# Kernel tuning notes

Measured on AMD Instinct MI355X. Metric: run time of the kernel, lower is better.

The kernel has to match this reference:

```python
import jax, jax.numpy as jnp
import numpy as np

B, SI, ST, D = 2, 1024, 512, 2048
H, KV, HD = 16, 4, 128
E, F, TOPK = 8, 1024, 2
EPS = 1e-6


def _rms(x, w):
    x32 = x.astype(jnp.float32)
    y = x32 * jax.lax.rsqrt(jnp.mean(x32 * x32, axis=-1, keepdims=True) + EPS)
    return y.astype(x.dtype) * w


def _rope(x, cos, sin):
    # x: [B,S,h,HD]; cos/sin: [S,HD//2]. Complex-pair rotation (use_real=False path):
    # pairs (x[2i], x[2i+1]) treated as complex, multiplied by e^{i theta}.
    xr, xi = x[..., 0::2], x[..., 1::2]
    c = cos[None, :, None, :]
    s = sin[None, :, None, :]
    out_r = xr * c - xi * s
    out_i = xr * s + xi * c
    return jnp.stack([out_r, out_i], axis=-1).reshape(x.shape)


def setup_inputs() -> dict:
    key = jax.random.key(0)
    ks = jax.random.split(key, 12)
    def w(k, shape, fan_in):
        return jax.random.normal(k, shape, jnp.float32) * (fan_in ** -0.5)
    pos_i = np.arange(SI)[:, None].astype(np.float32)
    pos_t = np.arange(ST)[:, None].astype(np.float32)
    inv = (1.0 / (10000.0 ** (np.arange(0, HD, 2).astype(np.float32) / HD)))[None, :]
    return {
        'hidden_states': jax.random.normal(ks[0], (B, SI, D), jnp.float32),
        'encoder_hidden_states': jax.random.normal(ks[1], (B, ST, D), jnp.float32),
        'img_cos': jnp.asarray(np.cos(pos_i * inv), jnp.float32),
        'img_sin': jnp.asarray(np.sin(pos_i * inv), jnp.float32),
        'txt_cos': jnp.asarray(np.cos(pos_t * inv), jnp.float32),
        'txt_sin': jnp.asarray(np.sin(pos_t * inv), jnp.float32),
        'norm1_w': jnp.ones((D,), jnp.float32),
        'norm2_w': jnp.ones((D,), jnp.float32),
        'wq': w(ks[2], (D, H * HD), D),
        'wk': w(ks[3], (D, KV * HD), D),
        'wv': w(ks[4], (D, KV * HD), D),
        'wk_txt': w(ks[5], (D, KV * HD), D),
        'wv_txt': w(ks[6], (D, KV * HD), D),
        'wo': w(ks[7], (H * HD, D), H * HD),
        'q_norm_w': jnp.ones((HD,), jnp.float32),
        'k_norm_w': jnp.ones((HD,), jnp.float32),
        'added_k_norm_w': jnp.ones((HD,), jnp.float32),
        'router_w': w(ks[8], (D, E), D),
        'gate_up_proj': w(ks[9], (E, D, 2 * F), D),
        'down_proj': w(ks[10], (E, F, D), F),
    }


def reference(hidden_states, encoder_hidden_states, img_cos, img_sin, txt_cos, txt_sin,
              norm1_w, norm2_w, wq, wk, wv, wk_txt, wv_txt, wo,
              q_norm_w, k_norm_w, added_k_norm_w, router_w, gate_up_proj, down_proj):
    h = hidden_states
    # ---- cross-attn: image queries over concat(image, text) K/V, GQA + RoPE ----
    x = _rms(h, norm1_w)
    q = _rms((x @ wq).reshape(B, SI, H, HD), q_norm_w)
    k_img = _rms((x @ wk).reshape(B, SI, KV, HD), k_norm_w)
    v_img = (x @ wv).reshape(B, SI, KV, HD)
    q = _rope(q, img_cos, img_sin)
    k_img = _rope(k_img, img_cos, img_sin)
    k_txt = _rms((encoder_hidden_states @ wk_txt).reshape(B, ST, KV, HD), added_k_norm_w)
    k_txt = _rope(k_txt, txt_cos, txt_sin)
    v_txt = (encoder_hidden_states @ wv_txt).reshape(B, ST, KV, HD)
    k = jnp.concatenate([k_img, k_txt], axis=1)  # [B, SI+ST, KV, HD]
    v = jnp.concatenate([v_img, v_txt], axis=1)
    k = jnp.repeat(k, H // KV, axis=2)  # GQA repeat_interleave over heads
    v = jnp.repeat(v, H // KV, axis=2)
    scores = jnp.einsum('bqhd,bkhd->bhqk', q, k) * (HD ** -0.5)
    attn = jax.nn.softmax(scores.astype(jnp.float32), axis=-1).astype(q.dtype)
    o = jnp.einsum('bhqk,bkhd->bqhd', attn, v).reshape(B, SI, H * HD)
    h = h + o @ wo
    # ---- MoE: top-k router + packed SwiGLU experts ----
    xt = _rms(h, norm2_w).reshape(B * SI, D)
    probs = jax.nn.softmax((xt @ router_w).astype(jnp.float32), axis=-1)
    topv, topi = jax.lax.top_k(probs, TOPK)
    topv = topv / jnp.sum(topv, axis=-1, keepdims=True)
    wgt = jnp.sum(jax.nn.one_hot(topi, E, dtype=xt.dtype) * topv.astype(xt.dtype)[..., None], axis=1)  # [T,E]
    gate_up = jnp.einsum('td,edg->teg', xt, gate_up_proj)  # [T,E,2F]
    gate, up = gate_up[..., :F], gate_up[..., F:]
    act = jax.nn.silu(gate) * up
    eo = jnp.einsum('tef,efd->ted', act, down_proj)  # [T,E,D]
    moe_out = jnp.einsum('te,ted->td', wgt, eo).reshape(B, SI, D)
    return h + moe_out
```

## Files before the change

kernel.cpp:

```cpp
#include <hip/hip_runtime.h>


typedef __attribute__((ext_vector_type(8))) __bf16 bf16x8;
typedef __attribute__((ext_vector_type(8))) unsigned short u16x8;
typedef __attribute__((ext_vector_type(4))) float f32x4;

__device__ __forceinline__ unsigned short f2bf(float x) {
  unsigned u = __builtin_bit_cast(unsigned, x);
  u += 0x7fffu + ((u >> 16) & 1u);
  return (unsigned short)(u >> 16);
}
__device__ __forceinline__ float bf2f(unsigned short b) {
  return __builtin_bit_cast(float, ((unsigned)b) << 16);
}

__device__ __forceinline__ void glds16(const unsigned short* g, unsigned short* l) {
  __builtin_amdgcn_global_load_lds(
      (const __attribute__((address_space(1))) void*)g,
      (__attribute__((address_space(3))) void*)l, 16, 0, 0);
}

__device__ __forceinline__ int xcd_swz(int orig, int nwg) {
  int q = nwg >> 3, r = nwg & 7;
  int xcd = orig & 7, idx = orig >> 3;
  int base = (xcd < r) ? xcd * (q + 1) : r * (q + 1) + (xcd - r) * q;
  return base + idx;
}

struct CvtJobs {
  const float* src[8];
  unsigned short* dst[8];
  int K[8];
  int N[8];
  int off[9];
};

__global__ __launch_bounds__(256) void convert_all(CvtJobs jb)
{
  __shared__ unsigned short T[64][66];
  const int bid = blockIdx.x;
  int j = 0;
  #pragma unroll
  for (int i = 0; i < 8; ++i) if (bid >= jb.off[i + 1]) j = i + 1;
  const int local = bid - jb.off[j];
  const int K = jb.K[j], N = jb.N[j];
  const int kb = K >> 6, nb = N >> 6;
  const int kt = local % kb;
  const int rest = local / kb;
  const int nt = rest % nb, zi = rest / nb;
  const float* Wz = jb.src[j] + (size_t)zi * K * N;
  unsigned short* WTz = jb.dst[j] + (size_t)zi * K * N;
  const int k0 = kt * 64, n0 = nt * 64;
  const int tid = threadIdx.x;
  #pragma unroll
  for (int i = tid; i < 64 * 16; i += 256) {
    int k = i >> 4, n4 = (i & 15) * 4;
    float4 v = *(const float4*)&Wz[(size_t)(k0 + k) * N + n0 + n4];
    T[n4 + 0][k] = f2bf(v.x);
    T[n4 + 1][k] = f2bf(v.y);
    T[n4 + 2][k] = f2bf(v.z);
    T[n4 + 3][k] = f2bf(v.w);
  }
  __syncthreads();
  #pragma unroll
  for (int i = tid; i < 64 * 8; i += 256) {
    int n = i >> 3, k8 = (i & 7) * 8;
    *(u16x8*)&WTz[(size_t)(n0 + n) * K + k0 + k8] = *(const u16x8*)&T[n][k8];
  }
}

struct Epi {
  unsigned short* qb;
  unsigned short* kbuf;
  unsigned short* vbuf;
  const float* q_nw;
  const float* k_nw;
  const float* kt_nw;
  const float* icos;
  const float* isin;
  const float* tcos;
  const float* tsin;
  float scale;
};

__global__ __launch_bounds__(256) void gemm_bb(
    const unsigned short* __restrict__ A, const unsigned short* __restrict__ BT,
    float* __restrict__ C, const float* __restrict__ resid,
    int M, int N, int K, int mode, Epi ep)
{
  __shared__ unsigned short As[2][128 * 64];
  __shared__ unsigned short Bs[2][128 * 64];
  const int mb = M >> 7;
  const int w = xcd_swz(blockIdx.x, gridDim.x);
  const int bm = (w % mb) * 128, bn = (w / mb) * 128;
  const int tid = threadIdx.x, lane = tid & 63, wid = tid >> 6;
  const int wm = (wid >> 1) * 64, wn = (wid & 1) * 64;
  const int l16 = lane & 15, g4 = lane >> 4;
  const int rseg = lane >> 3;
  const int csw  = ((lane & 7) ^ rseg) * 8;
  const unsigned short* aSrc[4];
  const unsigned short* bSrc[4];
  #pragma unroll
  for (int p = 0; p < 4; ++p) {
    int row = (p * 4 + wid) * 8 + rseg;
    aSrc[p] = A  + (size_t)(bm + row) * K + csw;
    bSrc[p] = BT + (size_t)(bn + row) * K + csw;
  }
  f32x4 acc[4][4] = {};
  const int NT = K >> 6;
  #pragma unroll
  for (int p = 0; p < 4; ++p) glds16(aSrc[p], &As[0][(p * 4 + wid) * 512]);
  #pragma unroll
  for (int p = 0; p < 4; ++p) glds16(bSrc[p], &Bs[0][(p * 4 + wid) * 512]);
  for (int t = 0; t < NT; ++t) {
    const int cur = t & 1;
    if (t + 1 < NT) {
      const int k0 = (t + 1) << 6;
      #pragma unroll
      for (int p = 0; p < 4; ++p) glds16(aSrc[p] + k0, &As[cur ^ 1][(p * 4 + wid) * 512]);
      #pragma unroll
      for (int p = 0; p < 4; ++p) glds16(bSrc[p] + k0, &Bs[cur ^ 1][(p * 4 + wid) * 512]);
      asm volatile("s_waitcnt vmcnt(8)" ::: "memory");
    } else {
      asm volatile("s_waitcnt vmcnt(0)" ::: "memory");
    }
    __builtin_amdgcn_s_barrier();
    __builtin_amdgcn_sched_barrier(0);
    const unsigned short* ab = &As[cur][0];
    const unsigned short* bb = &Bs[cur][0];
    #pragma unroll
    for (int ks = 0; ks < 2; ++ks) {
      bf16x8 af[4], bf[4];
      #pragma unroll
      for (int i = 0; i < 4; ++i) {
        int ra = wm + i * 16 + l16;
        int rb = wn + i * 16 + l16;
        int ch = ((ks * 4 + g4) ^ (l16 & 7)) * 8;
        af[i] = *(const bf16x8*)&ab[ra * 64 + ch];
        bf[i] = *(const bf16x8*)&bb[rb * 64 + ch];
      }
      #pragma unroll
      for (int mi = 0; mi < 4; ++mi)
        #pragma unroll
        for (int ni = 0; ni < 4; ++ni)
          acc[mi][ni] = __builtin_amdgcn_mfma_f32_16x16x32_bf16(af[mi], bf[ni], acc[mi][ni], 0, 0, 0);
    }
    __builtin_amdgcn_sched_barrier(0);
    __builtin_amdgcn_s_barrier();
  }
  const int r4 = g4 * 4;

  if (mode == 0) {
    #pragma unroll
    for (int mi = 0; mi < 4; ++mi)
      #pragma unroll
      for (int ni = 0; ni < 4; ++ni)
        #pragma unroll
        for (int r = 0; r < 4; ++r) {
          int row = bm + wm + mi * 16 + r4 + r;
          int col = bn + wn + ni * 16 + l16;
          float v = acc[mi][ni][r];
          if (resid) v += resid[(size_t)row * N + col];
          C[(size_t)row * N + col] = v;
        }
    return;
  }

  const int bt = bn >> 7;
  unsigned short* dst;
  const float* nw = nullptr;
  const float* cosT = nullptr;
  const float* sinT = nullptr;
  int h, NH, st, soff, vkind = 0, shift;
  float premul = 1.f;
  int S;
  if (mode == 1) {
    S = 1024; shift = 10;
    if (bt < 16)      { h = bt;      dst = ep.qb;   nw = ep.q_nw; cosT = ep.icos; sinT = ep.isin;
                        NH = 16; st = 1024; soff = 0; premul = ep.scale; }
    else if (bt < 20) { h = bt - 16; dst = ep.kbuf; nw = ep.k_nw; cosT = ep.icos; sinT = ep.isin;
                        NH = 4;  st = 1536; soff = 0; }
    else              { h = bt - 20; dst = ep.vbuf; vkind = 1; NH = 4; st = 1536; soff = 0; }
  } else {
    S = 512; shift = 9;
    if (bt < 4) { h = bt;     dst = ep.kbuf; nw = ep.kt_nw; cosT = ep.tcos; sinT = ep.tsin;
                  NH = 4; st = 1536; soff = 1024; }
    else        { h = bt - 4; dst = ep.vbuf; vkind = 1; NH = 4; st = 1536; soff = 1024; }
  }

  if (vkind) {
    #pragma unroll
    for (int mi = 0; mi < 4; ++mi)
      #pragma unroll
      for (int ni = 0; ni < 4; ++ni)
        #pragma unroll
        for (int r = 0; r < 4; ++r) {
          int row = wm + mi * 16 + r4 + r;
          int d   = wn + ni * 16 + l16;
          int token = bm + row;
          int srow = token & (S - 1), bidx = token >> shift;
          dst[((size_t)(bidx * NH + h) * st + srow + soff) * 128 + d] = f2bf(acc[mi][ni][r]);
        }
    return;
  }

  float* ssb = (float*)&As[0][0];
  float ssp[4][4];
  #pragma unroll
  for (int mi = 0; mi < 4; ++mi)
    #pragma unroll
    for (int r = 0; r < 4; ++r) {
      float v = 0.f;
      #pragma unroll
      for (int ni = 0; ni < 4; ++ni) v += acc[mi][ni][r] * acc[mi][ni][r];
      #pragma unroll
      for (int off = 1; off < 16; off <<= 1) v += __shfl_xor(v, off);
      ssp[mi][r] = v;
    }
  __syncthreads();
  if (l16 == 0) {
    #pragma unroll
    for (int mi = 0; mi < 4; ++mi)
      #pragma unroll
      for (int r = 0; r < 4; ++r)
        ssb[(wid & 1) * 128 + wm + mi * 16 + r4 + r] = ssp[mi][r];
  }
  __syncthreads();
  #pragma unroll
  for (int mi = 0; mi < 4; ++mi)
    #pragma unroll
    for (int r = 0; r < 4; ++r) {
      int row = wm + mi * 16 + r4 + r;
      float tot = ssb[row] + ssb[128 + row];
      float inv = rsqrtf(tot * (1.f / 128.f) + 1e-6f);
      int token = bm + row;
      int srow = token & (S - 1), bidx = token >> shift;
      #pragma unroll
      for (int ni = 0; ni < 4; ++ni) {
        int d = wn + ni * 16 + l16;
        float y = acc[mi][ni][r] * inv * nw[d];
        float part = __shfl_xor(y, 1);
        float c  = cosT[srow * 64 + (d >> 1)];
        float sn = sinT[srow * 64 + (d >> 1)];
        float outv = (d & 1) ? (part * sn + y * c) : (y * c - part * sn);
        dst[((size_t)(bidx * NH + h) * st + srow + soff) * 128 + d] = f2bf(outv * premul);
      }
    }
}

__global__ __launch_bounds__(512, 1) void gemm_moe_256sk(
    const unsigned short* __restrict__ A, const unsigned short* __restrict__ BTall,
    float* __restrict__ C0, float* __restrict__ C1,
    const int* __restrict__ counts, const int* __restrict__ offsets,
    const int* __restrict__ pair_token, const unsigned short* __restrict__ zbuf,
    int gather, int K, int N)
{
  const int w = xcd_swz(blockIdx.x, gridDim.x);
  const int e = w >> 7;
  const int local = w & 127;
  const int bm = ((local >> 4) & 7) * 256;
  const int kh = (local >> 3) & 1;
  const int bn = (local & 7) * 256;
  const int cnt = counts[e];
  if (bm >= cnt) return;
  const int base = offsets[e];
  const int Kh = K >> 1;
  float* __restrict__ C = kh ? C1 : C0;
  __shared__ unsigned short As[256 * 64];
  __shared__ unsigned short Bs[256 * 64];
  __shared__ int rowmap[256];
  const int tid = threadIdx.x, lane = tid & 63, wid = tid >> 6;
  const int wr = wid >> 2, wc = wid & 3;
  const int l16 = lane & 15, g4 = lane >> 4;
  const int rseg = lane >> 3;
  const int csw  = ((lane & 7) ^ rseg) * 8;
  if (tid < 256) {
    int lr = bm + tid;
    rowmap[tid] = (lr < cnt) ? (gather ? pair_token[base + lr] : base + lr) : -1;
  }
  __syncthreads();
  const unsigned short* BT = BTall + (size_t)e * N * K;
  const unsigned short* aSrc[4];
  const unsigned short* bSrc[4];
  int aOk[4];
  #pragma unroll
  for (int p = 0; p < 4; ++p) {
    int row = (p * 8 + wid) * 8 + rseg;
    int tok = rowmap[row];
    aOk[p] = (tok >= 0);
    aSrc[p] = aOk[p] ? (A + (size_t)tok * K + kh * Kh + csw) : (zbuf + csw);
    bSrc[p] = BT + (size_t)(bn + row) * K + kh * Kh + csw;
  }
  f32x4 acc[8][4] = {};
  const int NT = Kh >> 6;
  for (int t = 0; t < NT; ++t) {
    const int k0 = t << 6;
    #pragma unroll
    for (int p = 0; p < 4; ++p)
      glds16(aSrc[p] + (aOk[p] ? k0 : 0), &As[(p * 8 + wid) * 512]);
    #pragma unroll
    for (int p = 0; p < 4; ++p)
      glds16(bSrc[p] + k0, &Bs[(p * 8 + wid) * 512]);
    __syncthreads();
    #pragma unroll
    for (int ks = 0; ks < 2; ++ks) {
      const int ch = ((ks * 4 + g4) ^ (l16 & 7)) * 8;
      bf16x8 bf[4];
      #pragma unroll
      for (int j = 0; j < 4; ++j)
        bf[j] = *(const bf16x8*)&Bs[(wc * 64 + j * 16 + l16) * 64 + ch];
      #pragma unroll
      for (int mi = 0; mi < 8; ++mi) {
        bf16x8 af = *(const bf16x8*)&As[(wr * 128 + mi * 16 + l16) * 64 + ch];
        #pragma unroll
        for (int ni = 0; ni < 4; ++ni)
          acc[mi][ni] = __builtin_amdgcn_mfma_f32_16x16x32_bf16(af, bf[ni], acc[mi][ni], 0, 0, 0);
      }
    }
    __syncthreads();
  }
  const int r4 = g4 * 4;
  #pragma unroll
  for (int mi = 0; mi < 8; ++mi)
    #pragma unroll
    for (int ni = 0; ni < 4; ++ni)
      #pragma unroll
      for (int r = 0; r < 4; ++r) {
        int lrow = bm + wr * 128 + mi * 16 + r4 + r;
        int col  = bn + wc * 64 + ni * 16 + l16;
        if (lrow < cnt)
          C[(size_t)(base + lrow) * N + col] = acc[mi][ni][r];
      }
}

__global__ __launch_bounds__(256) void rmsnorm_rows(
    const float* __restrict__ in, const float* __restrict__ w,
    unsigned short* __restrict__ out)
{
  const int row = blockIdx.x;
  const int tid = threadIdx.x;
  const float* x = in + (size_t)row * 2048;
  float4 a = *(const float4*)&x[tid * 8];
  float4 b = *(const float4*)&x[tid * 8 + 4];
  float s = a.x*a.x + a.y*a.y + a.z*a.z + a.w*a.w
          + b.x*b.x + b.y*b.y + b.z*b.z + b.w*b.w;
  #pragma unroll
  for (int off = 1; off < 64; off <<= 1) s += __shfl_xor(s, off);
  __shared__ float red[4];
  if ((tid & 63) == 0) red[tid >> 6] = s;
  __syncthreads();
  float inv = rsqrtf((red[0] + red[1] + red[2] + red[3]) * (1.f / 2048.f) + 1e-6f);
  float4 wa = *(const float4*)&w[tid * 8];
  float4 wb = *(const float4*)&w[tid * 8 + 4];
  unsigned short* o = out + (size_t)row * 2048 + tid * 8;
  o[0] = f2bf(a.x * inv * wa.x); o[1] = f2bf(a.y * inv * wa.y);
  o[2] = f2bf(a.z * inv * wa.z); o[3] = f2bf(a.w * inv * wa.w);
  o[4] = f2bf(b.x * inv * wb.x); o[5] = f2bf(b.y * inv * wb.y);
  o[6] = f2bf(b.z * inv * wb.z); o[7] = f2bf(b.w * inv * wb.w);
}

__global__ __launch_bounds__(256) void rmsnorm_router(
    const float* __restrict__ in, const float* __restrict__ w,
    unsigned short* __restrict__ xt, const float* __restrict__ rw,
    int* __restrict__ topi, float* __restrict__ topw, int* __restrict__ counts)
{
  const int row = blockIdx.x;
  const int tid = threadIdx.x, lane = tid & 63, wid = tid >> 6;
  const float* x = in + (size_t)row * 2048;
  float4 a = *(const float4*)&x[tid * 8];
  float4 b = *(const float4*)&x[tid * 8 + 4];
  float s = a.x*a.x + a.y*a.y + a.z*a.z + a.w*a.w
          + b.x*b.x + b.y*b.y + b.z*b.z + b.w*b.w;
  #pragma unroll
  for (int off = 1; off < 64; off <<= 1) s += __shfl_xor(s, off);
  __shared__ float red[4];
  __shared__ float rl[4][8];
  if (lane == 0) red[wid] = s;
  __syncthreads();
  float inv = rsqrtf((red[0] + red[1] + red[2] + red[3]) * (1.f / 2048.f) + 1e-6f);
  float4 wa = *(const float4*)&w[tid * 8];
  float4 wb = *(const float4*)&w[tid * 8 + 4];
  float y[8] = {a.x * inv * wa.x, a.y * inv * wa.y, a.z * inv * wa.z, a.w * inv * wa.w,
                b.x * inv * wb.x, b.y * inv * wb.y, b.z * inv * wb.z, b.w * inv * wb.w};
  unsigned short* o = xt + (size_t)row * 2048 + tid * 8;
  #pragma unroll
  for (int j = 0; j < 8; ++j) o[j] = f2bf(y[j]);
  float lg[8] = {};
  #pragma unroll
  for (int j = 0; j < 8; ++j) {
    int d = tid * 8 + j;
    const float4 r0 = *(const float4*)&rw[d * 8];
    const float4 r1 = *(const float4*)&rw[d * 8 + 4];
    lg[0] += y[j] * r0.x; lg[1] += y[j] * r0.y; lg[2] += y[j] * r0.z; lg[3] += y[j] * r0.w;
    lg[4] += y[j] * r1.x; lg[5] += y[j] * r1.y; lg[6] += y[j] * r1.z; lg[7] += y[j] * r1.w;
  }
  #pragma unroll
  for (int e = 0; e < 8; ++e)
    #pragma unroll
    for (int off = 1; off < 64; off <<= 1) lg[e] += __shfl_xor(lg[e], off);
  if (lane == 0) {
    #pragma unroll
    for (int e = 0; e < 8; ++e) rl[wid][e] = lg[e];
  }
  __syncthreads();
  if (tid == 0) {
    float l[8];
    #pragma unroll
    for (int e = 0; e < 8; ++e) l[e] = rl[0][e] + rl[1][e] + rl[2][e] + rl[3][e];
    float v0 = l[0]; int e0 = 0;
    #pragma unroll
    for (int e = 1; e < 8; ++e) if (l[e] > v0) { v0 = l[e]; e0 = e; }
    float v1 = -1e30f; int e1 = 0;
    #pragma unroll
    for (int e = 0; e < 8; ++e) if (e != e0 && l[e] > v1) { v1 = l[e]; e1 = e; }
    float x1 = expf(v1 - v0);
    float w0 = 1.f / (1.f + x1);
    float w1 = x1 / (1.f + x1);
    topi[2 * row] = e0; topi[2 * row + 1] = e1;
    topw[2 * row] = w0; topw[2 * row + 1] = w1;
    atomicAdd(&counts[e0], 1);
    atomicAdd(&counts[e1], 1);
  }
}

__global__ __launch_bounds__(256) void f32_to_bf16_k(
    const float* __restrict__ in, unsigned short* __restrict__ out, int n)
{
  int i = (blockIdx.x * 256 + threadIdx.x) * 4;
  if (i + 3 < n) {
    float4 v = *(const float4*)&in[i];
    out[i + 0] = f2bf(v.x); out[i + 1] = f2bf(v.y);
    out[i + 2] = f2bf(v.z); out[i + 3] = f2bf(v.w);
  }
}

__global__ __launch_bounds__(512) void attn_kernel(
    const unsigned short* __restrict__ q,
    const unsigned short* __restrict__ kbuf,
    const unsigned short* __restrict__ vbuf,
    unsigned short* __restrict__ o)
{
  const int SK = 1536;
  const int w = xcd_swz(blockIdx.x, gridDim.x);
  const int bh = w >> 3;
  const int b = bh >> 4, h = bh & 15, kvh = h >> 2;
  const int q0 = (w & 7) * 128;
  const int tid = threadIdx.x, lane = tid & 63, wid = tid >> 6;
  const int l16 = lane & 15, kb = (lane >> 4) * 8, r4 = (lane >> 4) * 4;
  __shared__ unsigned short KsL[64 * 128];
  __shared__ unsigned short VTL[128 * 64];
  __shared__ unsigned short PsL[8 * 16 * 64];
  const int sr0 = tid >> 4;
  const int scc = (tid & 15) * 8;

  const unsigned short* qrow =
      q + ((size_t)(b * 16 + h) * 1024 + q0 + wid * 16 + l16) * 128;
  bf16x8 qf[4];
  #pragma unroll
  for (int ks = 0; ks < 4; ++ks) qf[ks] = *(const bf16x8*)&qrow[ks * 32 + kb];
  float mrow[4] = {-1e30f, -1e30f, -1e30f, -1e30f};
  float lrow[4] = {0.f, 0.f, 0.f, 0.f};
  f32x4 oacc[8] = {};
  const unsigned short* kb_base = kbuf + (size_t)(b * 4 + kvh) * SK * 128;
  const unsigned short* vb_base = vbuf + (size_t)(b * 4 + kvh) * SK * 128;

  u16x8 k0[2], v0[2], k1[2], v1[2];

#define ATT_LOAD(kr, vr, kt1)                                                 \
  {                                                                           \
    _Pragma("unroll")                                                         \
    for (int i = 0; i < 2; ++i) {                                             \
      kr[i] = *(const u16x8*)&kb_base[(size_t)((kt1) + sr0 + 32 * i) * 128 + scc]; \
      vr[i] = *(const u16x8*)&vb_base[(size_t)((kt1) + sr0 + 32 * i) * 128 + scc]; \
    }                                                                         \
  }

#define ATT_STAGE(kr, vr)                                                     \
  {                                                                           \
    _Pragma("unroll")                                                         \
    for (int i = 0; i < 2; ++i) {                                             \
      int rr = sr0 + 32 * i;                                                  \
      *(u16x8*)&KsL[rr * 128 + (((scc >> 3) ^ (rr & 7)) << 3)] = kr[i];       \
      _Pragma("unroll")                                                       \
      for (int j = 0; j < 8; ++j)                                             \
        VTL[(scc + j) * 64 + ((((rr >> 3) ^ ((scc + j) >> 3)) & 7) << 3) + (rr & 7)] = vr[i][j]; \
    }                                                                         \
  }

  auto compute = [&]() {
    f32x4 sacc[4] = {};
    __builtin_amdgcn_s_setprio(1);
    #pragma unroll
    for (int ks = 0; ks < 4; ++ks) {
      #pragma unroll
      for (int ni = 0; ni < 4; ++ni) {
        int rr = ni * 16 + l16;
        bf16x8 kf = *(const bf16x8*)
            &KsL[rr * 128 + ((((ks * 32 + kb) >> 3) ^ (rr & 7)) << 3)];
        sacc[ni] = __builtin_amdgcn_mfma_f32_16x16x32_bf16(qf[ks], kf, sacc[ni], 0, 0, 0);
      }
    }
    __builtin_amdgcn_s_setprio(0);
    float pv[4][4], alpha[4];
    #pragma unroll
    for (int r = 0; r < 4; ++r) {
      float tm = fmaxf(fmaxf(sacc[0][r], sacc[1][r]), fmaxf(sacc[2][r], sacc[3][r]));
      #pragma unroll
      for (int off = 1; off < 16; off <<= 1) tm = fmaxf(tm, __shfl_xor(tm, off));
      float mn = fmaxf(mrow[r], tm);
      alpha[r] = __expf(mrow[r] - mn);
      float s = 0.f;
      #pragma unroll
      for (int ni = 0; ni < 4; ++ni) {
        float p = __expf(sacc[ni][r] - mn);
        pv[ni][r] = p; s += p;
      }
      #pragma unroll
      for (int off = 1; off < 16; off <<= 1) s += __shfl_xor(s, off);
      lrow[r] = lrow[r] * alpha[r] + s;
      mrow[r] = mn;
    }
    #pragma unroll
    for (int ni = 0; ni < 8; ++ni)
      #pragma unroll
      for (int r = 0; r < 4; ++r) oacc[ni][r] *= alpha[r];
    #pragma unroll
    for (int ni = 0; ni < 4; ++ni)
      #pragma unroll
      for (int r = 0; r < 4; ++r) {
        int row = r4 + r, col = ni * 16 + l16;
        PsL[wid * 1024 + row * 64 + ((((col >> 3) ^ (row & 7)) & 7) << 3) + (col & 7)]
            = f2bf(pv[ni][r]);
      }
    asm volatile("s_waitcnt lgkmcnt(0)" ::: "memory");
    __builtin_amdgcn_sched_barrier(0);
    __builtin_amdgcn_s_setprio(1);
    #pragma unroll
    for (int ks = 0; ks < 2; ++ks) {
      bf16x8 pf = *(const bf16x8*)
          &PsL[wid * 1024 + l16 * 64 + ((((ks * 32 + kb) >> 3) ^ (l16 & 7)) << 3)];
      #pragma unroll
      for (int ni = 0; ni < 8; ++ni) {
        int d = ni * 16 + l16;
        bf16x8 vf = *(const bf16x8*)
            &VTL[d * 64 + ((((ks * 32 + kb) >> 3) ^ ((d >> 3) & 7)) << 3)];
        oacc[ni] = __builtin_amdgcn_mfma_f32_16x16x32_bf16(pf, vf, oacc[ni], 0, 0, 0);
      }
    }
    __builtin_amdgcn_s_setprio(0);
  };

  ATT_LOAD(k0, v0, 0);
  for (int t = 0; t < 24; t += 2) {
    ATT_STAGE(k0, v0);
    ATT_LOAD(k1, v1, (t + 1) * 64);
    asm volatile("s_waitcnt lgkmcnt(0)" ::: "memory");
    __builtin_amdgcn_s_barrier();
    __builtin_amdgcn_sched_barrier(0);
    compute();
    __builtin_amdgcn_sched_barrier(0);
    __builtin_amdgcn_s_barrier();
    ATT_STAGE(k1, v1);
    if (t + 2 < 24) ATT_LOAD(k0, v0, (t + 2) * 64);
    asm volatile("s_waitcnt lgkmcnt(0)" ::: "memory");
    __builtin_amdgcn_s_barrier();
    __builtin_amdgcn_sched_barrier(0);
    compute();
    __builtin_amdgcn_sched_barrier(0);
    __builtin_amdgcn_s_barrier();
  }
#undef ATT_LOAD
#undef ATT_STAGE

  #pragma unroll
  for (int ni = 0; ni < 8; ++ni)
    #pragma unroll
    for (int r = 0; r < 4; ++r) {
      float val = oacc[ni][r] / lrow[r];
      size_t row = (size_t)b * 1024 + q0 + wid * 16 + r4 + r;
      o[row * 2048 + h * 128 + ni * 16 + l16] = f2bf(val);
    }
}

__global__ void scan_offsets(const int* __restrict__ counts, int* __restrict__ offsets)
{
  if (threadIdx.x == 0 && blockIdx.x == 0) {
    int a = 0;
    for (int e = 0; e < 8; ++e) { offsets[e] = a; a += counts[e]; }
    offsets[8] = a;
  }
}

__global__ __launch_bounds__(256) void scatter_pairs(
    const int* __restrict__ topi, const int* __restrict__ offsets,
    int* __restrict__ fill, int* __restrict__ pair_token, int* __restrict__ token_slot)
{
  int t = blockIdx.x * 256 + threadIdx.x;
  if (t >= 2048) return;
  #pragma unroll
  for (int k = 0; k < 2; ++k) {
    int e = topi[2 * t + k];
    int slot = offsets[e] + atomicAdd(&fill[e], 1);
    pair_token[slot] = t;
    token_slot[2 * t + k] = slot;
  }
}

__global__ __launch_bounds__(256) void act_silu2(
    const float* __restrict__ gu0, const float* __restrict__ gu1,
    unsigned short* __restrict__ act)
{
  int p = blockIdx.x;
  int c = threadIdx.x * 4;
  float4 g0 = *(const float4*)&gu0[(size_t)p * 2048 + c];
  float4 g1 = *(const float4*)&gu1[(size_t)p * 2048 + c];
  float4 u0 = *(const float4*)&gu0[(size_t)p * 2048 + 1024 + c];
  float4 u1 = *(const float4*)&gu1[(size_t)p * 2048 + 1024 + c];
  float gg[4] = {g0.x + g1.x, g0.y + g1.y, g0.z + g1.z, g0.w + g1.w};
  float uu[4] = {u0.x + u1.x, u0.y + u1.y, u0.z + u1.z, u0.w + u1.w};
  #pragma unroll
  for (int j = 0; j < 4; ++j) {
    float a = gg[j] / (1.f + __expf(-gg[j])) * uu[j];
    act[(size_t)p * 1024 + c + j] = f2bf(a);
  }
}

__global__ __launch_bounds__(256) void moe_combine2(
    float* __restrict__ out, const float* __restrict__ eo0,
    const float* __restrict__ eo1,
    const int* __restrict__ token_slot, const float* __restrict__ topw)
{
  int t = blockIdx.x;
  int c = threadIdx.x * 8;
  int s0 = token_slot[2 * t], s1 = token_slot[2 * t + 1];
  float w0 = topw[2 * t], w1 = topw[2 * t + 1];
  #pragma unroll
  for (int j0 = 0; j0 < 8; j0 += 4) {
    float4 a0 = *(const float4*)&eo0[(size_t)s0 * 2048 + c + j0];
    float4 a1 = *(const float4*)&eo1[(size_t)s0 * 2048 + c + j0];
    float4 b0 = *(const float4*)&eo0[(size_t)s1 * 2048 + c + j0];
    float4 b1 = *(const float4*)&eo1[(size_t)s1 * 2048 + c + j0];
    float4 v = *(const float4*)&out[(size_t)t * 2048 + c + j0];
    v.x += w0 * (a0.x + a1.x) + w1 * (b0.x + b1.x);
    v.y += w0 * (a0.y + a1.y) + w1 * (b0.y + b1.y);
    v.z += w0 * (a0.z + a1.z) + w1 * (b0.z + b1.z);
    v.w += w0 * (a0.w + a1.w) + w1 * (b0.w + b1.w);
    *(float4*)&out[(size_t)t * 2048 + c + j0] = v;
  }
}

extern "C" void kernel_launch(void* const* d_in, const int* in_sizes, int n_in,
                              void* d_out, int out_size, void* d_ws, size_t ws_size,
                              hipStream_t stream)
{
  const float* hidden  = (const float*)d_in[0];
  const float* enc     = (const float*)d_in[1];
  const float* img_cos = (const float*)d_in[2];
  const float* img_sin = (const float*)d_in[3];
  const float* txt_cos = (const float*)d_in[4];
  const float* txt_sin = (const float*)d_in[5];
  const float* norm1_w = (const float*)d_in[6];
  const float* norm2_w = (const float*)d_in[7];
  const float* wq      = (const float*)d_in[8];
  const float* wk      = (const float*)d_in[9];
  const float* wv      = (const float*)d_in[10];
  const float* wk_txt  = (const float*)d_in[11];
  const float* wv_txt  = (const float*)d_in[12];
  const float* wo      = (const float*)d_in[13];
  const float* q_norm_w       = (const float*)d_in[14];
  const float* k_norm_w       = (const float*)d_in[15];
  const float* added_k_norm_w = (const float*)d_in[16];
  const float* router_w       = (const float*)d_in[17];
  const float* gate_up_proj   = (const float*)d_in[18];
  const float* down_proj      = (const float*)d_in[19];
  float* out = (float*)d_out;

  char* ws = (char*)d_ws;
  size_t off = 0;
  auto alloc = [&](size_t bytes) {
    void* p = ws + off;
    off += (bytes + 255) & ~(size_t)255;
    return p;
  };
  unsigned short* wqkvT  = (unsigned short*)alloc(3072ULL * 2048 * 2);
  unsigned short* wkvtT  = (unsigned short*)alloc(1024ULL * 2048 * 2);
  unsigned short* woT    = (unsigned short*)alloc(2048ULL * 2048 * 2);
  unsigned short* gupT   = (unsigned short*)alloc(8ULL * 2048 * 2048 * 2);
  unsigned short* dnT    = (unsigned short*)alloc(8ULL * 2048 * 1024 * 2);
  unsigned short* x_bf   = (unsigned short*)alloc(2048ULL * 2048 * 2);
  unsigned short* enc_bf = (unsigned short*)alloc(1024ULL * 2048 * 2);
  float* gu0  = (float*)alloc(4096ULL * 2048 * 4);
  float* gu1  = (float*)alloc(4096ULL * 2048 * 4);
  unsigned short* qb   = (unsigned short*)alloc(2048ULL * 2048 * 2);
  unsigned short* kbuf = (unsigned short*)alloc(2ULL * 4 * 1536 * 128 * 2);
  unsigned short* vbuf = (unsigned short*)alloc(2ULL * 4 * 1536 * 128 * 2);
  unsigned short* obuf = (unsigned short*)alloc(2048ULL * 2048 * 2);
  unsigned short* act  = obuf;
  unsigned short* xt   = (unsigned short*)alloc(2048ULL * 2048 * 2);
  int*   ctrl  = (int*)alloc(64 * sizeof(int));
  int*   topi  = (int*)alloc(4096 * 4);
  float* topw  = (float*)alloc(4096 * 4);
  int*   tslot = (int*)alloc(4096 * 4);
  int*   ptok  = (int*)alloc(4096 * 4);
  unsigned short* zbuf = (unsigned short*)alloc(256);
  int* counts = ctrl, * fill = ctrl + 8, * offsets = ctrl + 16;

  hipMemsetAsync(ctrl, 0, 64, stream);
  hipMemsetAsync(zbuf, 0, 256, stream);

  const float scale = 0.08838834764831845f;

  CvtJobs jb;
  jb.src[0] = wq;     jb.dst[0] = wqkvT;                  jb.K[0] = 2048; jb.N[0] = 2048;
  jb.src[1] = wk;     jb.dst[1] = wqkvT + 2048ULL * 2048; jb.K[1] = 2048; jb.N[1] = 512;
  jb.src[2] = wv;     jb.dst[2] = wqkvT + 2560ULL * 2048; jb.K[2] = 2048; jb.N[2] = 512;
  jb.src[3] = wk_txt; jb.dst[3] = wkvtT;                  jb.K[3] = 2048; jb.N[3] = 512;
  jb.src[4] = wv_txt; jb.dst[4] = wkvtT + 512ULL * 2048;  jb.K[4] = 2048; jb.N[4] = 512;
  jb.src[5] = wo;     jb.dst[5] = woT;                    jb.K[5] = 2048; jb.N[5] = 2048;
  jb.src[6] = gate_up_proj; jb.dst[6] = gupT;             jb.K[6] = 2048; jb.N[6] = 2048;
  jb.src[7] = down_proj;    jb.dst[7] = dnT;              jb.K[7] = 1024; jb.N[7] = 2048;
  jb.off[0] = 0;     jb.off[1] = 1024;  jb.off[2] = 1280; jb.off[3] = 1536;
  jb.off[4] = 1792;  jb.off[5] = 2048;  jb.off[6] = 3072; jb.off[7] = 11264;
  jb.off[8] = 15360;
  convert_all<<<15360, 256, 0, stream>>>(jb);

  rmsnorm_rows<<<2048, 256, 0, stream>>>(hidden, norm1_w, x_bf);
  f32_to_bf16_k<<<2048, 256, 0, stream>>>(enc, enc_bf, 1024 * 2048);

  Epi ep;
  ep.qb = qb; ep.kbuf = kbuf; ep.vbuf = vbuf;
  ep.q_nw = q_norm_w; ep.k_nw = k_norm_w; ep.kt_nw = added_k_norm_w;
  ep.icos = img_cos; ep.isin = img_sin; ep.tcos = txt_cos; ep.tsin = txt_sin;
  ep.scale = scale;

  gemm_bb<<<384, 256, 0, stream>>>(x_bf, wqkvT, nullptr, nullptr, 2048, 3072, 2048, 1, ep);
  gemm_bb<<<64, 256, 0, stream>>>(enc_bf, wkvtT, nullptr, nullptr, 1024, 1024, 2048, 2, ep);

  attn_kernel<<<256, 512, 0, stream>>>(qb, kbuf, vbuf, obuf);

  gemm_bb<<<256, 256, 0, stream>>>(obuf, woT, out, hidden, 2048, 2048, 2048, 0, ep);

  rmsnorm_router<<<2048, 256, 0, stream>>>(out, norm2_w, xt, router_w,
                                           topi, topw, counts);
  scan_offsets<<<1, 64, 0, stream>>>(counts, offsets);
  scatter_pairs<<<8, 256, 0, stream>>>(topi, offsets, fill, ptok, tslot);

  gemm_moe_256sk<<<1024, 512, 0, stream>>>(xt, gupT, gu0, gu1,
                                           counts, offsets, ptok, zbuf, 1, 2048, 2048);
  act_silu2<<<4096, 256, 0, stream>>>(gu0, gu1, act);
  gemm_moe_256sk<<<1024, 512, 0, stream>>>(act, dnT, gu0, gu1,
                                           counts, offsets, ptok, zbuf, 0, 1024, 2048);
  moe_combine2<<<2048, 256, 0, stream>>>(out, gu0, gu1, tslot, topw);
}
```

Measured before the change: 558.7 us.

## Double-buffer MoE GEMM loads, store bf16 partials, fuse small prep kernels

The MoE GEMM now prefetches the next K tile into a second LDS buffer while computing the current one, using explicit vmcnt waits and raw barriers in place of two __syncthreads. Its split-K partial outputs are written as bf16 instead of fp32, which halves the traffic into act_silu2 and moe_combine2 at some cost in precision. The input norm and encoder conversion are merged into one launch, and the scan and scatter routing kernels become a single one-block kernel using shared-memory atomics. Doubling the LDS buffers raises shared memory per block, and the hand-set vmcnt count depends on how many loads each thread issues.

Measured after the change: 512.7 us. -8.2%, faster.

```diff
diff --git a/kernel.cpp b/kernel.cpp
--- a/kernel.cpp
+++ b/kernel.cpp
@@ -3,6 +3,7 @@
 
 typedef __attribute__((ext_vector_type(8))) __bf16 bf16x8;
 typedef __attribute__((ext_vector_type(8))) unsigned short u16x8;
+typedef __attribute__((ext_vector_type(4))) unsigned short u16x4;
 typedef __attribute__((ext_vector_type(4))) float f32x4;
 
 __device__ __forceinline__ unsigned short f2bf(float x) {
@@ -250,7 +251,7 @@
 
 __global__ __launch_bounds__(512, 1) void gemm_moe_256sk(
     const unsigned short* __restrict__ A, const unsigned short* __restrict__ BTall,
-    float* __restrict__ C0, float* __restrict__ C1,
+    unsigned short* __restrict__ C0, unsigned short* __restrict__ C1,
     const int* __restrict__ counts, const int* __restrict__ offsets,
     const int* __restrict__ pair_token, const unsigned short* __restrict__ zbuf,
     int gather, int K, int N)
@@ -265,9 +266,9 @@
   if (bm >= cnt) return;
   const int base = offsets[e];
   const int Kh = K >> 1;
-  float* __restrict__ C = kh ? C1 : C0;
-  __shared__ unsigned short As[256 * 64];
-  __shared__ unsigned short Bs[256 * 64];
+  unsigned short* __restrict__ C = kh ? C1 : C0;
+  __shared__ unsigned short As[2][256 * 64];
+  __shared__ unsigned short Bs[2][256 * 64];
   __shared__ int rowmap[256];
   const int tid = threadIdx.x, lane = tid & 63, wid = tid >> 6;
   const int wr = wid >> 2, wc = wid & 3;
@@ -293,31 +294,45 @@
   }
   f32x4 acc[8][4] = {};
   const int NT = Kh >> 6;
+  #pragma unroll
+  for (int p = 0; p < 4; ++p) glds16(aSrc[p], &As[0][(p * 8 + wid) * 512]);
+  #pragma unroll
+  for (int p = 0; p < 4; ++p) glds16(bSrc[p], &Bs[0][(p * 8 + wid) * 512]);
   for (int t = 0; t < NT; ++t) {
-    const int k0 = t << 6;
-    #pragma unroll
-    for (int p = 0; p < 4; ++p)
-      glds16(aSrc[p] + (aOk[p] ? k0 : 0), &As[(p * 8 + wid) * 512]);
-    #pragma unroll
-    for (int p = 0; p < 4; ++p)
-      glds16(bSrc[p] + k0, &Bs[(p * 8 + wid) * 512]);
-    __syncthreads();
+    const int cur = t & 1;
+    if (t + 1 < NT) {
+      const int k0 = (t + 1) << 6;
+      #pragma unroll
+      for (int p = 0; p < 4; ++p)
+        glds16(aSrc[p] + (aOk[p] ? k0 : 0), &As[cur ^ 1][(p * 8 + wid) * 512]);
+      #pragma unroll
+      for (int p = 0; p < 4; ++p)
+        glds16(bSrc[p] + k0, &Bs[cur ^ 1][(p * 8 + wid) * 512]);
+      asm volatile("s_waitcnt vmcnt(8)" ::: "memory");
+    } else {
+      asm volatile("s_waitcnt vmcnt(0)" ::: "memory");
+    }
+    __builtin_amdgcn_s_barrier();
+    __builtin_amdgcn_sched_barrier(0);
+    const unsigned short* ab = &As[cur][0];
+    const unsigned short* bb = &Bs[cur][0];
     #pragma unroll
     for (int ks = 0; ks < 2; ++ks) {
       const int ch = ((ks * 4 + g4) ^ (l16 & 7)) * 8;
       bf16x8 bf[4];
       #pragma unroll
       for (int j = 0; j < 4; ++j)
-        bf[j] = *(const bf16x8*)&Bs[(wc * 64 + j * 16 + l16) * 64 + ch];
+        bf[j] = *(const bf16x8*)&bb[(wc * 64 + j * 16 + l16) * 64 + ch];
       #pragma unroll
       for (int mi = 0; mi < 8; ++mi) {
-        bf16x8 af = *(const bf16x8*)&As[(wr * 128 + mi * 16 + l16) * 64 + ch];
+        bf16x8 af = *(const bf16x8*)&ab[(wr * 128 + mi * 16 + l16) * 64 + ch];
         #pragma unroll
         for (int ni = 0; ni < 4; ++ni)
           acc[mi][ni] = __builtin_amdgcn_mfma_f32_16x16x32_bf16(af, bf[ni], acc[mi][ni], 0, 0, 0);
       }
     }
-    __syncthreads();
+    __builtin_amdgcn_sched_barrier(0);
+    __builtin_amdgcn_s_barrier();
   }
   const int r4 = g4 * 4;
   #pragma unroll
@@ -329,17 +344,28 @@
         int lrow = bm + wr * 128 + mi * 16 + r4 + r;
         int col  = bn + wc * 64 + ni * 16 + l16;
         if (lrow < cnt)
-          C[(size_t)(base + lrow) * N + col] = acc[mi][ni][r];
+          C[(size_t)(base + lrow) * N + col] = f2bf(acc[mi][ni][r]);
       }
 }
 
-__global__ __launch_bounds__(256) void rmsnorm_rows(
-    const float* __restrict__ in, const float* __restrict__ w,
-    unsigned short* __restrict__ out)
+__global__ __launch_bounds__(256) void pre_norm(
+    const float* __restrict__ hidden, const float* __restrict__ w,
+    unsigned short* __restrict__ x_bf,
+    const float* __restrict__ enc, unsigned short* __restrict__ enc_bf)
 {
   const int row = blockIdx.x;
   const int tid = threadIdx.x;
-  const float* x = in + (size_t)row * 2048;
+  if (row >= 2048) {
+    const int r = row - 2048;
+    const float* x = enc + (size_t)r * 2048 + tid * 8;
+    unsigned short* o = enc_bf + (size_t)r * 2048 + tid * 8;
+    float4 a = *(const float4*)&x[0];
+    float4 b = *(const float4*)&x[4];
+    o[0] = f2bf(a.x); o[1] = f2bf(a.y); o[2] = f2bf(a.z); o[3] = f2bf(a.w);
+    o[4] = f2bf(b.x); o[5] = f2bf(b.y); o[6] = f2bf(b.z); o[7] = f2bf(b.w);
+    return;
+  }
+  const float* x = hidden + (size_t)row * 2048;
   float4 a = *(const float4*)&x[tid * 8];
   float4 b = *(const float4*)&x[tid * 8 + 4];
   float s = a.x*a.x + a.y*a.y + a.z*a.z + a.w*a.w
@@ -352,7 +378,7 @@
   float inv = rsqrtf((red[0] + red[1] + red[2] + red[3]) * (1.f / 2048.f) + 1e-6f);
   float4 wa = *(const float4*)&w[tid * 8];
   float4 wb = *(const float4*)&w[tid * 8 + 4];
-  unsigned short* o = out + (size_t)row * 2048 + tid * 8;
+  unsigned short* o = x_bf + (size_t)row * 2048 + tid * 8;
   o[0] = f2bf(a.x * inv * wa.x); o[1] = f2bf(a.y * inv * wa.y);
   o[2] = f2bf(a.z * inv * wa.z); o[3] = f2bf(a.w * inv * wa.w);
   o[4] = f2bf(b.x * inv * wb.x); o[5] = f2bf(b.y * inv * wb.y);
@@ -423,14 +449,31 @@
   }
 }
 
-__global__ __launch_bounds__(256) void f32_to_bf16_k(
-    const float* __restrict__ in, unsigned short* __restrict__ out, int n)
-{
-  int i = (blockIdx.x * 256 + threadIdx.x) * 4;
-  if (i + 3 < n) {
-    float4 v = *(const float4*)&in[i];
-    out[i + 0] = f2bf(v.x); out[i + 1] = f2bf(v.y);
-    out[i + 2] = f2bf(v.z); out[i + 3] = f2bf(v.w);
+__global__ __launch_bounds__(256) void route_build(
+    const int* __restrict__ counts, int* __restrict__ offsets,
+    const int* __restrict__ topi,
+    int* __restrict__ pair_token, int* __restrict__ token_slot)
+{
+  __shared__ int soff[9];
+  __shared__ int sfill[8];
+  const int tid = threadIdx.x;
+  if (tid == 0) {
+    int a = 0;
+    #pragma unroll
+    for (int e = 0; e < 8; ++e) { soff[e] = a; a += counts[e]; }
+    soff[8] = a;
+  }
+  if (tid < 8) sfill[tid] = 0;
+  __syncthreads();
+  if (tid < 9) offsets[tid] = soff[tid];
+  for (int t = tid; t < 2048; t += 256) {
+    #pragma unroll
+    for (int k = 0; k < 2; ++k) {
+      int e = topi[2 * t + k];
+      int slot = soff[e] + atomicAdd(&sfill[e], 1);
+      pair_token[slot] = t;
+      token_slot[2 * t + k] = slot;
+    }
   }
 }
 
@@ -582,69 +625,45 @@
     }
 }
 
-__global__ void scan_offsets(const int* __restrict__ counts, int* __restrict__ offsets)
-{
-  if (threadIdx.x == 0 && blockIdx.x == 0) {
-    int a = 0;
-    for (int e = 0; e < 8; ++e) { offsets[e] = a; a += counts[e]; }
-    offsets[8] = a;
-  }
-}
-
-__global__ __launch_bounds__(256) void scatter_pairs(
-    const int* __restrict__ topi, const int* __restrict__ offsets,
-    int* __restrict__ fill, int* __restrict__ pair_token, int* __restrict__ token_slot)
-{
-  int t = blockIdx.x * 256 + threadIdx.x;
-  if (t >= 2048) return;
-  #pragma unroll
-  for (int k = 0; k < 2; ++k) {
-    int e = topi[2 * t + k];
-    int slot = offsets[e] + atomicAdd(&fill[e], 1);
-    pair_token[slot] = t;
-    token_slot[2 * t + k] = slot;
-  }
-}
-
 __global__ __launch_bounds__(256) void act_silu2(
-    const float* __restrict__ gu0, const float* __restrict__ gu1,
+    const unsigned short* __restrict__ gu0, const unsigned short* __restrict__ gu1,
     unsigned short* __restrict__ act)
 {
   int p = blockIdx.x;
   int c = threadIdx.x * 4;
-  float4 g0 = *(const float4*)&gu0[(size_t)p * 2048 + c];
-  float4 g1 = *(const float4*)&gu1[(size_t)p * 2048 + c];
-  float4 u0 = *(const float4*)&gu0[(size_t)p * 2048 + 1024 + c];
-  float4 u1 = *(const float4*)&gu1[(size_t)p * 2048 + 1024 + c];
-  float gg[4] = {g0.x + g1.x, g0.y + g1.y, g0.z + g1.z, g0.w + g1.w};
-  float uu[4] = {u0.x + u1.x, u0.y + u1.y, u0.z + u1.z, u0.w + u1.w};
+  u16x4 g0 = *(const u16x4*)&gu0[(size_t)p * 2048 + c];
+  u16x4 g1 = *(const u16x4*)&gu1[(size_t)p * 2048 + c];
+  u16x4 u0 = *(const u16x4*)&gu0[(size_t)p * 2048 + 1024 + c];
+  u16x4 u1 = *(const u16x4*)&gu1[(size_t)p * 2048 + 1024 + c];
   #pragma unroll
   for (int j = 0; j < 4; ++j) {
-    float a = gg[j] / (1.f + __expf(-gg[j])) * uu[j];
+    float g = bf2f(g0[j]) + bf2f(g1[j]);
+    float u = bf2f(u0[j]) + bf2f(u1[j]);
+    float a = g / (1.f + __expf(-g)) * u;
     act[(size_t)p * 1024 + c + j] = f2bf(a);
   }
 }
 
 __global__ __launch_bounds__(256) void moe_combine2(
-    float* __restrict__ out, const float* __restrict__ eo0,
-    const float* __restrict__ eo1,
+    float* __restrict__ out, const unsigned short* __restrict__ eo0,
+    const unsigned short* __restrict__ eo1,
     const int* __restrict__ token_slot, const float* __restrict__ topw)
 {
   int t = blockIdx.x;
   int c = threadIdx.x * 8;
   int s0 = token_slot[2 * t], s1 = token_slot[2 * t + 1];
   float w0 = topw[2 * t], w1 = topw[2 * t + 1];
+  u16x8 a0 = *(const u16x8*)&eo0[(size_t)s0 * 2048 + c];
+  u16x8 a1 = *(const u16x8*)&eo1[(size_t)s0 * 2048 + c];
+  u16x8 b0 = *(const u16x8*)&eo0[(size_t)s1 * 2048 + c];
+  u16x8 b1 = *(const u16x8*)&eo1[(size_t)s1 * 2048 + c];
   #pragma unroll
   for (int j0 = 0; j0 < 8; j0 += 4) {
-    float4 a0 = *(const float4*)&eo0[(size_t)s0 * 2048 + c + j0];
-    float4 a1 = *(const float4*)&eo1[(size_t)s0 * 2048 + c + j0];
-    float4 b0 = *(const float4*)&eo0[(size_t)s1 * 2048 + c + j0];
-    float4 b1 = *(const float4*)&eo1[(size_t)s1 * 2048 + c + j0];
     float4 v = *(const float4*)&out[(size_t)t * 2048 + c + j0];
-    v.x += w0 * (a0.x + a1.x) + w1 * (b0.x + b1.x);
-    v.y += w0 * (a0.y + a1.y) + w1 * (b0.y + b1.y);
-    v.z += w0 * (a0.z + a1.z) + w1 * (b0.z + b1.z);
-    v.w += w0 * (a0.w + a1.w) + w1 * (b0.w + b1.w);
+    v.x += w0 * (bf2f(a0[j0+0]) + bf2f(a1[j0+0])) + w1 * (bf2f(b0[j0+0]) + bf2f(b1[j0+0]));
+    v.y += w0 * (bf2f(a0[j0+1]) + bf2f(a1[j0+1])) + w1 * (bf2f(b0[j0+1]) + bf2f(b1[j0+1]));
+    v.z += w0 * (bf2f(a0[j0+2]) + bf2f(a1[j0+2])) + w1 * (bf2f(b0[j0+2]) + bf2f(b1[j0+2]));
+    v.w += w0 * (bf2f(a0[j0+3]) + bf2f(a1[j0+3])) + w1 * (bf2f(b0[j0+3]) + bf2f(b1[j0+3]));
     *(float4*)&out[(size_t)t * 2048 + c + j0] = v;
   }
 }
@@ -689,8 +708,8 @@
   unsigned short* dnT    = (unsigned short*)alloc(8ULL * 2048 * 1024 * 2);
   unsigned short* x_bf   = (unsigned short*)alloc(2048ULL * 2048 * 2);
   unsigned short* enc_bf = (unsigned short*)alloc(1024ULL * 2048 * 2);
-  float* gu0  = (float*)alloc(4096ULL * 2048 * 4);
-  float* gu1  = (float*)alloc(4096ULL * 2048 * 4);
+  unsigned short* gu0 = (unsigned short*)alloc(4096ULL * 2048 * 2);
+  unsigned short* gu1 = (unsigned short*)alloc(4096ULL * 2048 * 2);
   unsigned short* qb   = (unsigned short*)alloc(2048ULL * 2048 * 2);
   unsigned short* kbuf = (unsigned short*)alloc(2ULL * 4 * 1536 * 128 * 2);
   unsigned short* vbuf = (unsigned short*)alloc(2ULL * 4 * 1536 * 128 * 2);
@@ -703,7 +722,7 @@
   int*   tslot = (int*)alloc(4096 * 4);
   int*   ptok  = (int*)alloc(4096 * 4);
   unsigned short* zbuf = (unsigned short*)alloc(256);
-  int* counts = ctrl, * fill = ctrl + 8, * offsets = ctrl + 16;
+  int* counts = ctrl, * offsets = ctrl + 16;
 
   hipMemsetAsync(ctrl, 0, 64, stream);
   hipMemsetAsync(zbuf, 0, 256, stream);
@@ -724,8 +743,7 @@
   jb.off[8] = 15360;
   convert_all<<<15360, 256, 0, stream>>>(jb);
 
-  rmsnorm_rows<<<2048, 256, 0, stream>>>(hidden, norm1_w, x_bf);
-  f32_to_bf16_k<<<2048, 256, 0, stream>>>(enc, enc_bf, 1024 * 2048);
+  pre_norm<<<3072, 256, 0, stream>>>(hidden, norm1_w, x_bf, enc, enc_bf);
 
   Epi ep;
   ep.qb = qb; ep.kbuf = kbuf; ep.vbuf = vbuf;
@@ -742,8 +760,7 @@
 
   rmsnorm_router<<<2048, 256, 0, stream>>>(out, norm2_w, xt, router_w,
                                            topi, topw, counts);
-  scan_offsets<<<1, 64, 0, stream>>>(counts, offsets);
-  scatter_pairs<<<8, 256, 0, stream>>>(topi, offsets, fill, ptok, tslot);
+  route_build<<<1, 256, 0, stream>>>(counts, offsets, topi, ptok, tslot);
 
   gemm_moe_256sk<<<1024, 512, 0, stream>>>(xt, gupT, gu0, gu1,
                                            counts, offsets, ptok, zbuf, 1, 2048, 2048);
```
